# Performance work log

Hardware: AMD Instinct MI355X
Metric: run time of the kernel (lower is better)

The kernel has to match this reference:

```python
import jax, jax.numpy as jnp
import numpy as np

HIDDEN = 1024
N_HEAD = 16
D_HEAD = HIDDEN // N_HEAD


def setup_inputs() -> dict:
    key = jax.random.key(0)
    k1, k2, k3, k4, k5, k6, k7 = jax.random.split(key, 7)
    B, Sq, Sk = 8, 1024, 1024
    decoder_input = jax.random.normal(k1, (B, Sq, HIDDEN), dtype=jnp.float32)
    encoder_output = jax.random.normal(k2, (B, Sk, HIDDEN), dtype=jnp.float32)
    # torch.rand -> uniform [0,1) for the per-head projection params
    W_query = jax.random.uniform(k3, (N_HEAD, D_HEAD, HIDDEN), dtype=jnp.float32)
    W_key = jax.random.uniform(k4, (N_HEAD, D_HEAD, HIDDEN), dtype=jnp.float32)
    W_value = jax.random.uniform(k5, (N_HEAD, D_HEAD, HIDDEN), dtype=jnp.float32)
    # nn.Linear default init: U(-1/sqrt(fan_in), 1/sqrt(fan_in))
    bound = 1.0 / np.sqrt(HIDDEN)
    W_out = jax.random.uniform(k6, (HIDDEN, HIDDEN), dtype=jnp.float32, minval=-bound, maxval=bound)
    b_out = jax.random.uniform(k7, (HIDDEN,), dtype=jnp.float32, minval=-bound, maxval=bound)
    return {
        "decoder_input": decoder_input,
        "encoder_output": encoder_output,
        "W_query": W_query,
        "W_key": W_key,
        "W_value": W_value,
        "W_out": W_out,
        "b_out": b_out,
    }


def reference(decoder_input, encoder_output, W_query, W_key, W_value, W_out, b_out):
    # per-head projections, vectorized over heads: x @ W[i].T == einsum over hidden
    q = jnp.einsum("bqh,ndh->bnqd", decoder_input, W_query)   # [B,N,Sq,D]
    k = jnp.einsum("bkh,ndh->bnkd", encoder_output, W_key)    # [B,N,Sk,D]
    v = jnp.einsum("bkh,ndh->bnkd", encoder_output, W_value)  # [B,N,Sk,D]
    scores = jnp.einsum("bnqd,bnkd->bnqk", q, k) / jnp.sqrt(jnp.float32(D_HEAD))
    attn = jax.nn.softmax(scores, axis=-1)                     # [B,N,Sq,Sk]
    heads = jnp.einsum("bnqk,bnkd->bnqd", attn, v)             # [B,N,Sq,D]
    B, N, Sq, D = heads.shape
    concat = jnp.transpose(heads, (0, 2, 1, 3)).reshape(B, Sq, N * D)  # [B,Sq,H]
    out = concat @ W_out.T + b_out
    return out
```

## Files before the change

### kernel.cpp

```cpp
#include <hip/hip_runtime.h>
#include <math.h>

#define HID 1024
#define NH 16
#define DH 64
#define BATCH 8
#define SEQ 1024
#define MTOT (BATCH * SEQ)

typedef __attribute__((ext_vector_type(8))) short bfrag;
typedef __attribute__((ext_vector_type(4))) float f32x4;
typedef __attribute__((ext_vector_type(8))) unsigned short us8;
typedef __attribute__((ext_vector_type(4))) unsigned short us4;
typedef unsigned int u32;
typedef unsigned short u16;

#define SCALE_Q 0.18033688011112042f

__device__ __forceinline__ u16 f2b(float f) {
    u32 u = __float_as_uint(f);
    return (u16)((u + 0x7FFFu + ((u >> 16) & 1u)) >> 16);
}
__device__ __forceinline__ float b2f(u16 h) { return __uint_as_float(((u32)h) << 16); }

__device__ __forceinline__ void gl_lds16(const void* g, void* l) {
    __builtin_amdgcn_global_load_lds(
        (const __attribute__((address_space(1))) unsigned int*)g,
        (__attribute__((address_space(3))) unsigned int*)l, 16, 0, 0);
}

__device__ __forceinline__ u32 swz(u32 L) { return L ^ (((L >> 6) & 7u) << 4); }
__device__ __forceinline__ u32 unswz(u32 p) {
    u32 b = ((((p >> 6) ^ (p >> 8)) & 1u) << 4) | (((p >> 7) & 1u) << 5) | (((p >> 8) & 1u) << 6);
    return p ^ b;
}
__device__ __forceinline__ u32 swz128(u32 L) { return L ^ (((L >> 7) & 7u) << 4); }

__global__ __launch_bounds__(256) void prep(
    const float* __restrict__ enc,
    const float* __restrict__ Wq, const float* __restrict__ Wk,
    const float* __restrict__ Wv, const float* __restrict__ Wo,
    u16* __restrict__ Eh,
    u16* __restrict__ Wqh, u16* __restrict__ Wql,
    u16* __restrict__ Wkh, u16* __restrict__ Wkl,
    u16* __restrict__ Wvh, u16* __restrict__ Woh)
{
    const int NX4 = MTOT * HID / 4;
    const int NW4 = HID * HID / 4;
    const int total = NX4 + 4 * NW4;
    for (int i = blockIdx.x * blockDim.x + threadIdx.x; i < total;
         i += gridDim.x * blockDim.x) {
        if (i < NX4) {
            float4 f = ((const float4*)enc)[i];
            us4 h;
            h[0] = f2b(f.x); h[1] = f2b(f.y); h[2] = f2b(f.z); h[3] = f2b(f.w);
            ((us4*)Eh)[i] = h;
        } else {
            int j = i - NX4;
            int rgn = j / NW4, k = j - rgn * NW4;
            const float* src = (rgn == 0) ? Wq : (rgn == 1) ? Wk : (rgn == 2) ? Wv : Wo;
            float4 f = ((const float4*)src)[k];
            float v[4] = {f.x, f.y, f.z, f.w};
            us4 h, l;
#pragma unroll
            for (int q = 0; q < 4; ++q) {
                u16 hh = f2b(v[q]);
                h[q] = hh;
                l[q] = f2b(v[q] - b2f(hh));
            }
            if (rgn == 0) { ((us4*)Wqh)[k] = h; ((us4*)Wql)[k] = l; }
            else if (rgn == 1) { ((us4*)Wkh)[k] = h; ((us4*)Wkl)[k] = l; }
            else if (rgn == 2) { ((us4*)Wvh)[k] = h; }
            else { ((us4*)Woh)[k] = h; }
        }
    }
}

template <int TERMS, int XMODE, int EPI>
__global__ __launch_bounds__(256) void gemm_mfma(
    const float* __restrict__ Xf, const u16* __restrict__ Xb,
    const u16* __restrict__ Wh, const u16* __restrict__ Wl,
    const float* __restrict__ bias, float scale,
    float* __restrict__ Of, u16* __restrict__ O1, u16* __restrict__ O2)
{
    constexpr u32 OFF_AH = 0, OFF_BH = 8192, OFF_AL = 16384, OFF_BL = 24576;
    __shared__ __align__(16) char smem[(TERMS == 3) ? 32768 : 16384];

    u32 bid = blockIdx.x;
    u32 wg = (bid & 7) * 64 + (bid >> 3);
    const u32 m0 = (wg >> 3) * 128, n0 = (wg & 7) * 128;

    const int tid = threadIdx.x;
    const int w = tid >> 6, lane = tid & 63, c = lane & 15, g = lane >> 4;
    const int wr = w >> 1, wc = w & 1;

    u32 pa[4], pb[4];
#pragma unroll
    for (int i = 0; i < 4; ++i) {
        pa[i] = swz((u32)(wr * 64 + i * 16 + c) * 64 + (u32)g * 16);
        pb[i] = swz((u32)(wc * 64 + i * 16 + c) * 64 + (u32)g * 16);
    }

    f32x4 acc[4][4];
#pragma unroll
    for (int i = 0; i < 4; ++i)
#pragma unroll
        for (int j = 0; j < 4; ++j) acc[i][j] = f32x4{0.f, 0.f, 0.f, 0.f};

    for (int kb = 0; kb < HID / 32; ++kb) {
        const int koff = kb * 32;
        {
            const int nB = (TERMS == 3) ? 16 : 8;
            const int total = nB + ((XMODE == 1) ? 8 : 0);
            for (int id = w; id < total; id += 4) {
                u32 p = (u32)(id & 7) * 1024 + (u32)lane * 16;
                u32 L = unswz(p);
                u32 row = L >> 6, colb = L & 63;
                const char* src;
                u32 loff;
                if (id < 8) {
                    src = (const char*)Wh + ((size_t)(n0 + row)) * 2048 + (size_t)koff * 2 + colb;
                    loff = OFF_BH + (p & 0xFFFFFC00u);
                } else if (TERMS == 3 && id < 16) {
                    src = (const char*)Wl + ((size_t)(n0 + row)) * 2048 + (size_t)koff * 2 + colb;
                    loff = OFF_BL + (p & 0xFFFFFC00u);
                } else {
                    src = (const char*)Xb + ((size_t)(m0 + row)) * 2048 + (size_t)koff * 2 + colb;
                    loff = OFF_AH + (p & 0xFFFFFC00u);
                }
                gl_lds16(src, smem + loff);
            }
        }
        if (XMODE == 0) {
            const int row = tid >> 1, half = tid & 1;
            const float* xr = Xf + ((size_t)(m0 + row)) * HID + koff + half * 16;
            float4 f0 = ((const float4*)xr)[0], f1 = ((const float4*)xr)[1],
                   f2 = ((const float4*)xr)[2], f3 = ((const float4*)xr)[3];
            float v[16] = {f0.x, f0.y, f0.z, f0.w, f1.x, f1.y, f1.z, f1.w,
                           f2.x, f2.y, f2.z, f2.w, f3.x, f3.y, f3.z, f3.w};
#pragma unroll
            for (int s = 0; s < 2; ++s) {
                us8 h, l8;
#pragma unroll
                for (int i = 0; i < 8; ++i) {
                    u16 hh = f2b(v[s * 8 + i]);
                    h[i] = hh;
                    if (TERMS == 3) l8[i] = f2b(v[s * 8 + i] - b2f(hh));
                }
                u32 ph = swz((u32)row * 64 + (u32)half * 32 + (u32)s * 16);
                *(us8*)(smem + OFF_AH + ph) = h;
                if (TERMS == 3) *(us8*)(smem + OFF_AL + ph) = l8;
            }
        }
        __syncthreads();
        bfrag ah[4], al[4];
#pragma unroll
        for (int mi = 0; mi < 4; ++mi) {
            ah[mi] = *(const bfrag*)(smem + OFF_AH + pa[mi]);
            if (TERMS == 3) al[mi] = *(const bfrag*)(smem + OFF_AL + pa[mi]);
        }
#pragma unroll
        for (int ni = 0; ni < 4; ++ni) {
            bfrag bh = *(const bfrag*)(smem + OFF_BH + pb[ni]);
            bfrag bl;
            if (TERMS == 3) bl = *(const bfrag*)(smem + OFF_BL + pb[ni]);
#pragma unroll
            for (int mi = 0; mi < 4; ++mi) {
                acc[mi][ni] = __builtin_amdgcn_mfma_f32_16x16x32_bf16(ah[mi], bh, acc[mi][ni], 0, 0, 0);
                if (TERMS == 3) {
                    acc[mi][ni] = __builtin_amdgcn_mfma_f32_16x16x32_bf16(ah[mi], bl, acc[mi][ni], 0, 0, 0);
                    acc[mi][ni] = __builtin_amdgcn_mfma_f32_16x16x32_bf16(al[mi], bh, acc[mi][ni], 0, 0, 0);
                }
            }
        }
        __syncthreads();
    }
#pragma unroll
    for (int mi = 0; mi < 4; ++mi) {
#pragma unroll
        for (int ni = 0; ni < 4; ++ni) {
            const u32 n = n0 + wc * 64 + ni * 16 + c;
            const u32 mb = m0 + wr * 64 + mi * 16 + 4 * g;
            if (EPI == 0) {
                float bv = bias[n];
#pragma unroll
                for (int r = 0; r < 4; ++r)
                    Of[(size_t)(mb + r) * HID + n] = acc[mi][ni][r] + bv;
            } else if (EPI == 2) {
                const u32 h = n >> 6, d = n & 63;
                const u32 b_ = mb >> 10, s = mb & 1023;
                size_t base = ((size_t)(b_ * NH + h) * SEQ + s) * 64 + d;
#pragma unroll
                for (int r = 0; r < 4; ++r) {
                    float v = acc[mi][ni][r] * scale;
                    u16 hh = f2b(v);
                    O1[base + (size_t)r * 64] = hh;
                    O2[base + (size_t)r * 64] = f2b(v - b2f(hh));
                }
            } else {
                const u32 h = n >> 6, d = n & 63;
                const u32 b_ = mb >> 10, s = mb & 1023;
                us4 o;
#pragma unroll
                for (int r = 0; r < 4; ++r) o[r] = f2b(acc[mi][ni][r]);
                *(us4*)&O1[((size_t)(b_ * NH + h) * 64 + d) * SEQ + s] = o;
            }
        }
    }
}

__global__ __launch_bounds__(256) void attn_mfma(
    const u16* __restrict__ Qh, const u16* __restrict__ Ql,
    const u16* __restrict__ Kh, const u16* __restrict__ Kl,
    const u16* __restrict__ Vt, u16* __restrict__ Cc)
{
    __shared__ __align__(16) u16 sQH[4096], sQL[4096], sKH[4096], sKL[4096], sVT[4096];
    __shared__ __align__(16) u16 sP[64 * 72];

    u32 bid = blockIdx.x;
    u32 wg = (bid & 7) * 256 + (bid >> 3);
    const int b = wg >> 8;
    const int head = (wg >> 4) & 15;
    const int q0 = (wg & 15) * 64;

    const int tid = threadIdx.x;
    const int w = tid >> 6, lane = tid & 63, c = lane & 15, g = lane >> 4;

    const size_t hb = (size_t)(b * NH + head);
    const char* gQH = (const char*)(Qh + (hb * SEQ + q0) * 64);
    const char* gQL = (const char*)(Ql + (hb * SEQ + q0) * 64);
    const char* gKH = (const char*)(Kh + hb * SEQ * 64);
    const char* gKL = (const char*)(Kl + hb * SEQ * 64);
    const char* gVT = (const char*)(Vt + hb * 64 * SEQ);

    for (int t = w; t < 16; t += 4) {
        u32 seg = (u32)(t & 7);
        u32 p = seg * 1024 + (u32)lane * 16;
        u32 ps = swz128(p);
        const char* src = ((t < 8) ? gQH : gQL) + ps;
        u16* dst = ((t < 8) ? sQH : sQL) + seg * 512;
        gl_lds16(src, dst);
    }

    float m_[4] = {-1e30f, -1e30f, -1e30f, -1e30f};
    float l_[4] = {0.f, 0.f, 0.f, 0.f};
    f32x4 acc[4];
#pragma unroll
    for (int j = 0; j < 4; ++j) acc[j] = f32x4{0.f, 0.f, 0.f, 0.f};

    for (int kc = 0; kc < SEQ / 64; ++kc) {
        __syncthreads();
        for (int t = w; t < 24; t += 4) {
            u32 seg = (u32)(t & 7);
            u32 p = seg * 1024 + (u32)lane * 16;
            u32 ps = swz128(p);
            const char* src;
            u16* dst;
            if (t < 8) {
                src = gKH + (size_t)kc * 8192 + ps;
                dst = sKH + seg * 512;
            } else if (t < 16) {
                src = gKL + (size_t)kc * 8192 + ps;
                dst = sKL + seg * 512;
            } else {
                u32 row = ps >> 7, col = ps & 127;
                src = gVT + (size_t)row * (SEQ * 2) + (size_t)kc * 128 + col;
                dst = sVT + seg * 512;
            }
            gl_lds16(src, dst);
        }
        __syncthreads();

        f32x4 s4[4];
#pragma unroll
        for (int j = 0; j < 4; ++j) s4[j] = f32x4{0.f, 0.f, 0.f, 0.f};
#pragma unroll
        for (int ks = 0; ks < 2; ++ks) {
            u32 aoff = swz128((u32)(w * 16 + c) * 128 + (u32)ks * 64 + (u32)g * 16);
            bfrag ah = *(const bfrag*)((const char*)sQH + aoff);
            bfrag al = *(const bfrag*)((const char*)sQL + aoff);
#pragma unroll
            for (int jf = 0; jf < 4; ++jf) {
                u32 boff = swz128((u32)(jf * 16 + c) * 128 + (u32)ks * 64 + (u32)g * 16);
                bfrag bh = *(const bfrag*)((const char*)sKH + boff);
                bfrag bl = *(const bfrag*)((const char*)sKL + boff);
                s4[jf] = __builtin_amdgcn_mfma_f32_16x16x32_bf16(ah, bh, s4[jf], 0, 0, 0);
                s4[jf] = __builtin_amdgcn_mfma_f32_16x16x32_bf16(ah, bl, s4[jf], 0, 0, 0);
                s4[jf] = __builtin_amdgcn_mfma_f32_16x16x32_bf16(al, bh, s4[jf], 0, 0, 0);
            }
        }

        float scl[4];
#pragma unroll
        for (int r = 0; r < 4; ++r) {
            float v0 = s4[0][r], v1 = s4[1][r], v2 = s4[2][r], v3 = s4[3][r];
            float rm = fmaxf(fmaxf(v0, v1), fmaxf(v2, v3));
            rm = fmaxf(rm, __shfl_xor(rm, 1));
            rm = fmaxf(rm, __shfl_xor(rm, 2));
            rm = fmaxf(rm, __shfl_xor(rm, 4));
            rm = fmaxf(rm, __shfl_xor(rm, 8));
            float mn = fmaxf(m_[r], rm);
            scl[r] = exp2f(m_[r] - mn);
            float p0 = exp2f(v0 - mn), p1 = exp2f(v1 - mn),
                  p2 = exp2f(v2 - mn), p3 = exp2f(v3 - mn);
            float rs = p0 + p1 + p2 + p3;
            rs += __shfl_xor(rs, 1);
            rs += __shfl_xor(rs, 2);
            rs += __shfl_xor(rs, 4);
            rs += __shfl_xor(rs, 8);
            l_[r] = l_[r] * scl[r] + rs;
            m_[r] = mn;
            const int prow = (w * 16 + 4 * g + r) * 72;
            sP[prow + 0 + c] = f2b(p0);
            sP[prow + 16 + c] = f2b(p1);
            sP[prow + 32 + c] = f2b(p2);
            sP[prow + 48 + c] = f2b(p3);
        }
#pragma unroll
        for (int jd = 0; jd < 4; ++jd) {
            f32x4 t = acc[jd];
            t[0] *= scl[0]; t[1] *= scl[1]; t[2] *= scl[2]; t[3] *= scl[3];
            acc[jd] = t;
        }

#pragma unroll
        for (int ks = 0; ks < 2; ++ks) {
            bfrag ap = *(const bfrag*)(sP + (w * 16 + c) * 72 + ks * 32 + g * 8);
#pragma unroll
            for (int jd = 0; jd < 4; ++jd) {
                u32 voff = swz128((u32)(jd * 16 + c) * 128 + (u32)ks * 64 + (u32)g * 16);
                bfrag bv = *(const bfrag*)((const char*)sVT + voff);
                acc[jd] = __builtin_amdgcn_mfma_f32_16x16x32_bf16(ap, bv, acc[jd], 0, 0, 0);
            }
        }
    }

    float inv[4] = {1.f / l_[0], 1.f / l_[1], 1.f / l_[2], 1.f / l_[3]};
#pragma unroll
    for (int jd = 0; jd < 4; ++jd) {
#pragma unroll
        for (int r = 0; r < 4; ++r) {
            Cc[((size_t)(b * SEQ + q0 + w * 16 + 4 * g + r)) * HID + head * DH + jd * 16 + c] =
                f2b(acc[jd][r] * inv[r]);
        }
    }
}

extern "C" void kernel_launch(void* const* d_in, const int* in_sizes, int n_in,
                              void* d_out, int out_size, void* d_ws, size_t ws_size,
                              hipStream_t stream)
{
    const float* dec = (const float*)d_in[0];
    const float* enc = (const float*)d_in[1];
    const float* Wq = (const float*)d_in[2];
    const float* Wk = (const float*)d_in[3];
    const float* Wv = (const float*)d_in[4];
    const float* Wo = (const float*)d_in[5];
    const float* bo = (const float*)d_in[6];
    float* out = (float*)d_out;

    char* ws = (char*)d_ws;
    const size_t MB = 1u << 20;
    u16* Eh  = (u16*)ws;
    u16* Qhg = (u16*)(ws + 16 * MB);
    u16* Qlg = (u16*)(ws + 32 * MB);
    u16* Khg = (u16*)(ws + 48 * MB);
    u16* Klg = (u16*)(ws + 64 * MB);
    u16* Vtg = (u16*)(ws + 80 * MB);
    u16* Wqh = (u16*)(ws + 96 * MB);
    u16* Wql = Wqh + (1u << 20);
    u16* Wkh = Wql + (1u << 20);
    u16* Wkl = Wkh + (1u << 20);
    u16* Wvh = Wkl + (1u << 20);
    u16* Woh = Wvh + (1u << 20);
    u16* Cc  = Eh;

    prep<<<2048, 256, 0, stream>>>(enc, Wq, Wk, Wv, Wo,
                                   Eh, Wqh, Wql, Wkh, Wkl, Wvh, Woh);

    gemm_mfma<3, 0, 2><<<512, 256, 0, stream>>>(dec, nullptr, Wqh, Wql, nullptr,
                                                SCALE_Q, nullptr, Qhg, Qlg);
    gemm_mfma<3, 0, 2><<<512, 256, 0, stream>>>(enc, nullptr, Wkh, Wkl, nullptr,
                                                1.0f, nullptr, Khg, Klg);
    gemm_mfma<1, 1, 3><<<512, 256, 0, stream>>>(nullptr, Eh, Wvh, nullptr, nullptr,
                                                1.0f, nullptr, Vtg, nullptr);

    attn_mfma<<<2048, 256, 0, stream>>>(Qhg, Qlg, Khg, Klg, Vtg, Cc);

    gemm_mfma<1, 1, 0><<<512, 256, 0, stream>>>(nullptr, Cc, Woh, nullptr, bo,
                                                1.0f, out, nullptr, nullptr);
}
```

Before: 462.1 us.

## Transpose attention MFMAs so each lane owns a query row, with lazy rescale

Swaps the MFMA operands so S^T and O^T are computed and each lane holds one query row. Softmax max and sum then reduce mostly within registers with only two cross-lane shuffles, and the running max is updated lazily, rescaling only when any lane's max grows by more than 8. It also keeps Q fragments in registers after the first chunk, precomputes K/V load pointers, writes P to a swizzled LDS buffer with packed bf16 stores, and stores the output as vectors. The aim is to cut shuffle, exp and rescale work in the softmax and the LDS traffic per iteration. The lazy threshold lets unnormalised values grow by up to 2^8, which is safe in fp32 but slightly changes bf16 rounding of P.

```diff
diff --git a/kernel.cpp b/kernel.cpp
--- a/kernel.cpp
+++ b/kernel.cpp
@@ -1,4 +1,5 @@
 #include <hip/hip_runtime.h>
+#include <hip/hip_bf16.h>
 #include <math.h>
 
 #define HID 1024
@@ -12,6 +13,7 @@
 typedef __attribute__((ext_vector_type(4))) float f32x4;
 typedef __attribute__((ext_vector_type(8))) unsigned short us8;
 typedef __attribute__((ext_vector_type(4))) unsigned short us4;
+typedef __attribute__((ext_vector_type(2))) unsigned int u32x2;
 typedef unsigned int u32;
 typedef unsigned short u16;
 
@@ -22,6 +24,13 @@
     return (u16)((u + 0x7FFFu + ((u >> 16) & 1u)) >> 16);
 }
 __device__ __forceinline__ float b2f(u16 h) { return __uint_as_float(((u32)h) << 16); }
+
+__device__ __forceinline__ u32 packbf(float a, float b) {
+    __hip_bfloat162 t = __float22bfloat162_rn(float2{a, b});
+    u32 r;
+    __builtin_memcpy(&r, &t, 4);
+    return r;
+}
 
 __device__ __forceinline__ void gl_lds16(const void* g, void* l) {
     __builtin_amdgcn_global_load_lds(
@@ -215,7 +224,7 @@
     const u16* __restrict__ Vt, u16* __restrict__ Cc)
 {
     __shared__ __align__(16) u16 sQH[4096], sQL[4096], sKH[4096], sKL[4096], sVT[4096];
-    __shared__ __align__(16) u16 sP[64 * 72];
+    __shared__ __align__(16) char sPw[8192];
 
     u32 bid = blockIdx.x;
     u32 wg = (bid & 7) * 256 + (bid >> 3);
@@ -235,114 +244,130 @@
 
     for (int t = w; t < 16; t += 4) {
         u32 seg = (u32)(t & 7);
-        u32 p = seg * 1024 + (u32)lane * 16;
-        u32 ps = swz128(p);
+        u32 ps = swz128(seg * 1024 + (u32)lane * 16);
         const char* src = ((t < 8) ? gQH : gQL) + ps;
         u16* dst = ((t < 8) ? sQH : sQL) + seg * 512;
         gl_lds16(src, dst);
     }
 
-    float m_[4] = {-1e30f, -1e30f, -1e30f, -1e30f};
-    float l_[4] = {0.f, 0.f, 0.f, 0.f};
+    const u32 ps0 = swz128((u32)w * 1024 + (u32)lane * 16);
+    const u32 ps1 = swz128((u32)(w + 4) * 1024 + (u32)lane * 16);
+    const char* pKH0 = gKH + ps0;  const char* pKH1 = gKH + ps1;
+    const char* pKL0 = gKL + ps0;  const char* pKL1 = gKL + ps1;
+    const char* pVT0 = gVT + (size_t)(ps0 >> 7) * (SEQ * 2) + (ps0 & 127);
+    const char* pVT1 = gVT + (size_t)(ps1 >> 7) * (SEQ * 2) + (ps1 & 127);
+    u16* dKH0 = sKH + w * 512;        u16* dKH1 = sKH + (w + 4) * 512;
+    u16* dKL0 = sKL + w * 512;        u16* dKL1 = sKL + (w + 4) * 512;
+    u16* dVT0 = sVT + w * 512;        u16* dVT1 = sVT + (w + 4) * 512;
+
+    char* pwBase = sPw + w * 2048;
+    const u32 pwRow = (u32)c * 128;
+    const u32 pwX = ((u32)(c & 7)) << 4;
+
+    float m_ = -1e30f, l_ = 0.f;
     f32x4 acc[4];
 #pragma unroll
     for (int j = 0; j < 4; ++j) acc[j] = f32x4{0.f, 0.f, 0.f, 0.f};
+    bfrag qh[2], ql[2];
 
     for (int kc = 0; kc < SEQ / 64; ++kc) {
         __syncthreads();
-        for (int t = w; t < 24; t += 4) {
-            u32 seg = (u32)(t & 7);
-            u32 p = seg * 1024 + (u32)lane * 16;
-            u32 ps = swz128(p);
-            const char* src;
-            u16* dst;
-            if (t < 8) {
-                src = gKH + (size_t)kc * 8192 + ps;
-                dst = sKH + seg * 512;
-            } else if (t < 16) {
-                src = gKL + (size_t)kc * 8192 + ps;
-                dst = sKL + seg * 512;
-            } else {
-                u32 row = ps >> 7, col = ps & 127;
-                src = gVT + (size_t)row * (SEQ * 2) + (size_t)kc * 128 + col;
-                dst = sVT + seg * 512;
-            }
-            gl_lds16(src, dst);
-        }
+        gl_lds16(pKH0, dKH0); gl_lds16(pKH1, dKH1);
+        gl_lds16(pKL0, dKL0); gl_lds16(pKL1, dKL1);
+        gl_lds16(pVT0, dVT0); gl_lds16(pVT1, dVT1);
+        pKH0 += 8192; pKH1 += 8192; pKL0 += 8192; pKL1 += 8192;
+        pVT0 += 128;  pVT1 += 128;
         __syncthreads();
 
+        if (kc == 0) {
+#pragma unroll
+            for (int ks = 0; ks < 2; ++ks) {
+                u32 aoff = swz128((u32)(w * 16 + c) * 128 + (u32)ks * 64 + (u32)g * 16);
+                qh[ks] = *(const bfrag*)((const char*)sQH + aoff);
+                ql[ks] = *(const bfrag*)((const char*)sQL + aoff);
+            }
+        }
+
         f32x4 s4[4];
 #pragma unroll
         for (int j = 0; j < 4; ++j) s4[j] = f32x4{0.f, 0.f, 0.f, 0.f};
 #pragma unroll
         for (int ks = 0; ks < 2; ++ks) {
-            u32 aoff = swz128((u32)(w * 16 + c) * 128 + (u32)ks * 64 + (u32)g * 16);
-            bfrag ah = *(const bfrag*)((const char*)sQH + aoff);
-            bfrag al = *(const bfrag*)((const char*)sQL + aoff);
 #pragma unroll
             for (int jf = 0; jf < 4; ++jf) {
-                u32 boff = swz128((u32)(jf * 16 + c) * 128 + (u32)ks * 64 + (u32)g * 16);
-                bfrag bh = *(const bfrag*)((const char*)sKH + boff);
-                bfrag bl = *(const bfrag*)((const char*)sKL + boff);
-                s4[jf] = __builtin_amdgcn_mfma_f32_16x16x32_bf16(ah, bh, s4[jf], 0, 0, 0);
-                s4[jf] = __builtin_amdgcn_mfma_f32_16x16x32_bf16(ah, bl, s4[jf], 0, 0, 0);
-                s4[jf] = __builtin_amdgcn_mfma_f32_16x16x32_bf16(al, bh, s4[jf], 0, 0, 0);
-            }
-        }
-
-        float scl[4];
-#pragma unroll
-        for (int r = 0; r < 4; ++r) {
-            float v0 = s4[0][r], v1 = s4[1][r], v2 = s4[2][r], v3 = s4[3][r];
-            float rm = fmaxf(fmaxf(v0, v1), fmaxf(v2, v3));
-            rm = fmaxf(rm, __shfl_xor(rm, 1));
-            rm = fmaxf(rm, __shfl_xor(rm, 2));
-            rm = fmaxf(rm, __shfl_xor(rm, 4));
-            rm = fmaxf(rm, __shfl_xor(rm, 8));
-            float mn = fmaxf(m_[r], rm);
-            scl[r] = exp2f(m_[r] - mn);
-            float p0 = exp2f(v0 - mn), p1 = exp2f(v1 - mn),
-                  p2 = exp2f(v2 - mn), p3 = exp2f(v3 - mn);
-            float rs = p0 + p1 + p2 + p3;
-            rs += __shfl_xor(rs, 1);
-            rs += __shfl_xor(rs, 2);
-            rs += __shfl_xor(rs, 4);
-            rs += __shfl_xor(rs, 8);
-            l_[r] = l_[r] * scl[r] + rs;
-            m_[r] = mn;
-            const int prow = (w * 16 + 4 * g + r) * 72;
-            sP[prow + 0 + c] = f2b(p0);
-            sP[prow + 16 + c] = f2b(p1);
-            sP[prow + 32 + c] = f2b(p2);
-            sP[prow + 48 + c] = f2b(p3);
-        }
-#pragma unroll
-        for (int jd = 0; jd < 4; ++jd) {
-            f32x4 t = acc[jd];
-            t[0] *= scl[0]; t[1] *= scl[1]; t[2] *= scl[2]; t[3] *= scl[3];
-            acc[jd] = t;
+                u32 koff = swz128((u32)(jf * 16 + c) * 128 + (u32)ks * 64 + (u32)g * 16);
+                bfrag kh_ = *(const bfrag*)((const char*)sKH + koff);
+                bfrag kl_ = *(const bfrag*)((const char*)sKL + koff);
+                s4[jf] = __builtin_amdgcn_mfma_f32_16x16x32_bf16(kh_, qh[ks], s4[jf], 0, 0, 0);
+                s4[jf] = __builtin_amdgcn_mfma_f32_16x16x32_bf16(kl_, qh[ks], s4[jf], 0, 0, 0);
+                s4[jf] = __builtin_amdgcn_mfma_f32_16x16x32_bf16(kh_, ql[ks], s4[jf], 0, 0, 0);
+            }
+        }
+
+        float pmax = s4[0][0];
+#pragma unroll
+        for (int jf = 0; jf < 4; ++jf)
+#pragma unroll
+            for (int r = 0; r < 4; ++r) pmax = fmaxf(pmax, s4[jf][r]);
+        pmax = fmaxf(pmax, __shfl_xor(pmax, 16));
+        pmax = fmaxf(pmax, __shfl_xor(pmax, 32));
+
+        if (!__all(pmax <= m_ + 8.f)) {
+            float mn = fmaxf(m_, pmax);
+            float scl = exp2f(m_ - mn);
+            m_ = mn;
+            l_ *= scl;
+#pragma unroll
+            for (int jd = 0; jd < 4; ++jd) {
+                f32x4 t = acc[jd];
+                t[0] *= scl; t[1] *= scl; t[2] *= scl; t[3] *= scl;
+                acc[jd] = t;
+            }
+        }
+
+        float p[16];
+        float rs = 0.f;
+#pragma unroll
+        for (int jf = 0; jf < 4; ++jf)
+#pragma unroll
+            for (int r = 0; r < 4; ++r) {
+                float pv = exp2f(s4[jf][r] - m_);
+                p[jf * 4 + r] = pv;
+                rs += pv;
+            }
+        rs += __shfl_xor(rs, 16);
+        rs += __shfl_xor(rs, 32);
+        l_ += rs;
+
+#pragma unroll
+        for (int jf = 0; jf < 4; ++jf) {
+            u32 w0 = packbf(p[jf * 4 + 0], p[jf * 4 + 1]);
+            u32 w1 = packbf(p[jf * 4 + 2], p[jf * 4 + 3]);
+            u32 off = (pwRow + (u32)(32 * jf + 8 * g)) ^ pwX;
+            *(u32x2*)(pwBase + off) = u32x2{w0, w1};
         }
 
 #pragma unroll
         for (int ks = 0; ks < 2; ++ks) {
-            bfrag ap = *(const bfrag*)(sP + (w * 16 + c) * 72 + ks * 32 + g * 8);
+            u32 roff = (pwRow + (u32)(64 * ks + 16 * g)) ^ pwX;
+            bfrag pf = *(const bfrag*)(pwBase + roff);
 #pragma unroll
             for (int jd = 0; jd < 4; ++jd) {
                 u32 voff = swz128((u32)(jd * 16 + c) * 128 + (u32)ks * 64 + (u32)g * 16);
-                bfrag bv = *(const bfrag*)((const char*)sVT + voff);
-                acc[jd] = __builtin_amdgcn_mfma_f32_16x16x32_bf16(ap, bv, acc[jd], 0, 0, 0);
-            }
-        }
-    }
-
-    float inv[4] = {1.f / l_[0], 1.f / l_[1], 1.f / l_[2], 1.f / l_[3]};
+                bfrag vv = *(const bfrag*)((const char*)sVT + voff);
+                acc[jd] = __builtin_amdgcn_mfma_f32_16x16x32_bf16(vv, pf, acc[jd], 0, 0, 0);
+            }
+        }
+    }
+
+    float inv = 1.f / l_;
+    size_t rowb = ((size_t)(b * SEQ + q0 + w * 16 + c)) * HID + head * DH;
 #pragma unroll
     for (int jd = 0; jd < 4; ++jd) {
-#pragma unroll
-        for (int r = 0; r < 4; ++r) {
-            Cc[((size_t)(b * SEQ + q0 + w * 16 + 4 * g + r)) * HID + head * DH + jd * 16 + c] =
-                f2b(acc[jd][r] * inv[r]);
-        }
+        us4 o;
+#pragma unroll
+        for (int r = 0; r < 4; ++r) o[r] = f2b(acc[jd][r] * inv);
+        *(us4*)&Cc[rowb + jd * 16 + 4 * g] = o;
     }
 }
 
```

After: 417.4 us. -9.7%, faster.
